# Optimization experiments

Hardware: AMD Instinct MI355X
Metric: run time of the kernel (lower is better)

Reference implementation:

```python
import jax, jax.numpy as jnp
import numpy as np

BN_EPS = 1e-5


def setup_inputs() -> dict:
    key = jax.random.key(0)
    ks = jax.random.split(key, 6)
    B, N, M, C1, C2 = 8, 8192, 2048, 128, 256
    in_ch = C1 + C2  # 384
    return {
        "xyz1": jax.random.uniform(ks[0], (B, N, 3), dtype=jnp.float32),
        "xyz2": jax.random.uniform(ks[1], (B, M, 3), dtype=jnp.float32),
        "features1": jax.random.normal(ks[2], (B, C1, N), dtype=jnp.float32),
        "features2": jax.random.normal(ks[3], (B, C2, M), dtype=jnp.float32),
        # Conv1d(kernel_size=1, bias=False) weights, squeezed to [out, in]
        "conv_w0": jax.random.normal(ks[4], (256, in_ch), dtype=jnp.float32) * 0.05,
        "gamma0": jnp.ones((256,), dtype=jnp.float32),
        "beta0": jnp.zeros((256,), dtype=jnp.float32),
        "conv_w1": jax.random.normal(ks[5], (256, 256), dtype=jnp.float32) * 0.05,
        "gamma1": jnp.ones((256,), dtype=jnp.float32),
        "beta1": jnp.zeros((256,), dtype=jnp.float32),
    }


def _conv_bn_relu(x, w, gamma, beta):
    # 1x1 Conv1d (no bias) == per-point channel matmul: [B,Cin,N] -> [B,Cout,N]
    x = jnp.einsum("oc,bcn->bon", w, x)
    # BatchNorm1d in training mode: batch stats over (B, N), biased variance
    mu = jnp.mean(x, axis=(0, 2), keepdims=True)
    var = jnp.var(x, axis=(0, 2), keepdims=True)
    x = (x - mu) * jax.lax.rsqrt(var + BN_EPS)
    x = x * gamma[None, :, None] + beta[None, :, None]
    return jax.nn.relu(x)


def reference(xyz1, xyz2, features1, features2,
              conv_w0, gamma0, beta0, conv_w1, gamma1, beta1):
    # squared pairwise distances [B, N, M] (broadcast diff reduced over coord dim)
    diff = xyz1[:, :, None, :] - xyz2[:, None, :, :]  # [B,N,M,3]
    dists = jnp.sum(diff * diff, axis=-1)             # [B,N,M]
    idx = jnp.argmin(dists, axis=-1)                  # [B,N] nearest downsampled point

    # per-batch gather: features2[b, :, idx[b]] -> [B, C2, N]
    interp = jax.vmap(lambda f, i: f[:, i])(features2, idx)

    x = jnp.concatenate([features1, interp], axis=1)  # [B, C1+C2, N]
    x = _conv_bn_relu(x, conv_w0, gamma0, beta0)
    x = _conv_bn_relu(x, conv_w1, gamma1, beta1)
    return x
```

## Files before the change

### kernel.cpp

```cpp
#include <hip/hip_runtime.h>
#include <stdint.h>

typedef unsigned short u16;
typedef unsigned int u32;
typedef __attribute__((ext_vector_type(8))) short short8;
typedef __attribute__((ext_vector_type(4))) float floatx4;

__device__ __forceinline__ u16 f2b(float f) {
  union { float f; u32 u; } c; c.f = f;
  u32 u = c.u;
  u += 0x7fffu + ((u >> 16) & 1u);
  return (u16)(u >> 16);
}
__device__ __forceinline__ float b2f(u16 h) {
  union { u32 u; float f; } c; c.u = ((u32)h) << 16;
  return c.f;
}

__device__ __forceinline__ void glds16(const void* g, void* l) {
  __builtin_amdgcn_global_load_lds((__attribute__((address_space(1))) void*)g,
                                   (__attribute__((address_space(3))) void*)l, 16, 0, 0);
}

__global__ void prep_all_k(const float* __restrict__ xyz1, const float* __restrict__ xyz2,
                           float2* __restrict__ cand,
                           const float* __restrict__ f1, u16* __restrict__ f1t,
                           const float* __restrict__ f2, u16* __restrict__ f2t,
                           const float* __restrict__ w0, u16* __restrict__ w0b,
                           const float* __restrict__ w1, u16* __restrict__ w1b,
                           float* __restrict__ sums) {
  __shared__ __align__(16) char smem[9216];
  int blk = blockIdx.x, t = threadIdx.x;
  if (blk < 512) {
    float4* s2 = (float4*)smem;
    int nq = blk & 7, mq = (blk >> 3) & 7, b = blk >> 6;
    const float* x2 = xyz2 + ((size_t)b * 2048 + mq * 256) * 3;
    s2[t] = make_float4(x2[t * 3], x2[t * 3 + 1], x2[t * 3 + 2], 0.f);
    __syncthreads();
    int n0 = nq * 1024 + t;
    float px[4], py[4], pz[4];
#pragma unroll
    for (int q = 0; q < 4; q++) {
      const float* p1 = xyz1 + ((size_t)b * 8192 + n0 + q * 256) * 3;
      px[q] = p1[0]; py[q] = p1[1]; pz[q] = p1[2];
    }
    float best[4] = {3.0e38f, 3.0e38f, 3.0e38f, 3.0e38f};
    int bi[4] = {0, 0, 0, 0};
#pragma unroll 4
    for (int m = 0; m < 256; m++) {
      float4 qq = s2[m];
#pragma unroll
      for (int q = 0; q < 4; q++) {
        float dx = px[q] - qq.x, dy = py[q] - qq.y, dz = pz[q] - qq.z;
        float d = fmaf(dz, dz, fmaf(dy, dy, dx * dx));
        bool c = d < best[q];
        best[q] = c ? d : best[q];
        bi[q] = c ? m : bi[q];
      }
    }
#pragma unroll
    for (int q = 0; q < 4; q++) {
      int n = n0 + q * 256;
      cand[(size_t)mq * 65536 + (size_t)b * 8192 + n] =
          make_float2(best[q], __int_as_float(mq * 256 + bi[q]));
    }
  } else if (blk < 3584) {
    const float* in; u16* out; int C, N, bx, by, bz;
    if (blk < 2560) { int rel = blk - 512;  in = f1; out = f1t; C = 128; N = 8192; bx = rel & 127; by = (rel >> 7) & 1; bz = rel >> 8; }
    else            { int rel = blk - 2560; in = f2; out = f2t; C = 256; N = 2048; bx = rel & 31;  by = (rel >> 5) & 3; bz = rel >> 7; }
    u16 (*tile)[72] = (u16(*)[72])smem;
    int c0 = by * 64, n0 = bx * 64;
    const float* src = in + ((size_t)bz * C + c0) * N + n0;
#pragma unroll
    for (int i = 0; i < 4; i++) {
      int id = t + i * 256;
      int c = id >> 4, nq = (id & 15) * 4;
      float4 v = *(const float4*)(src + (size_t)c * N + nq);
      tile[nq + 0][c] = f2b(v.x);
      tile[nq + 1][c] = f2b(v.y);
      tile[nq + 2][c] = f2b(v.z);
      tile[nq + 3][c] = f2b(v.w);
    }
    __syncthreads();
    int n = t >> 2, ch = (t & 3) * 16;
    u16* dst = out + ((size_t)bz * N + n0 + n) * C + c0 + ch;
    *(uint4*)dst = *(const uint4*)&tile[n][ch];
    *(uint4*)(dst + 8) = *(const uint4*)&tile[n][ch + 8];
  } else {
    int rel = blk - 3584;
    int i = rel * 256 + t;
    if (rel < 384) w0b[i] = f2b(w0[i]);
    else { int j = i - 98304; w1b[j] = f2b(w1[j]); }
    if (rel < 4) sums[i] = 0.f;
  }
}

__global__ __launch_bounds__(256, 2) void gemm1_k(const u16* __restrict__ w0b, const u16* __restrict__ f1t,
                                                  const u16* __restrict__ f2t, const float2* __restrict__ cand,
                                                  float* __restrict__ sum0, float* __restrict__ sq0,
                                                  u16* __restrict__ y0) {
  __shared__ u16 Bs[2][64 * 64];
  __shared__ float red[256];
  int t = threadIdx.x;
  int bid = blockIdx.x;
  int ohalf = (bid >> 3) & 1;
  int pairidx = (bid & 7) | ((bid >> 4) << 3);
  int o0 = ohalf * 128;
  int lane = t & 63, wave = t >> 6;
  int wrow = (wave >> 1) * 64;
  int wp = (wave & 1) * 32;
  int lr = lane & 15, lq = lane >> 4;
  int srow = lane >> 3;
  int sch = ((lane & 7) ^ srow) * 8;

  red[t] = 0.f;

  short8 areg[4][12];
#pragma unroll
  for (int i = 0; i < 4; i++) {
    const u16* wr = w0b + (size_t)(o0 + wrow + i * 16 + lr) * 384 + lq * 8;
#pragma unroll
    for (int kf = 0; kf < 12; kf++)
      areg[i][kf] = *(const short8*)(wr + kf * 32);
  }

  for (int s = 0; s < 4; s++) {
    int pt0 = (pairidx * 4 + s) * 64;
    size_t bb = (size_t)((pt0 >> 13) << 11);
    int gidx[2];
#pragma unroll
    for (int i = 0; i < 2; i++) {
      int p = pt0 + (wave * 2 + i) * 8 + srow;
      float bd = 3.0e38f; int bi = 0;
#pragma unroll
      for (int qc = 0; qc < 8; qc++) {
        float2 c = cand[(size_t)qc * 65536 + p];
        if (c.x < bd) { bd = c.x; bi = __float_as_int(c.y); }
      }
      gidx[i] = bi;
    }
    floatx4 zero = {0.f, 0.f, 0.f, 0.f};
    floatx4 acc[4][2];
#pragma unroll
    for (int i = 0; i < 4; i++)
#pragma unroll
      for (int j = 0; j < 2; j++) acc[i][j] = zero;

    auto stageB = [&](int step, int bufi) {
#pragma unroll
      for (int i = 0; i < 2; i++) {
        int row = (wave * 2 + i) * 8 + srow;
        const u16* src;
        if (step < 2) src = f1t + (size_t)(pt0 + row) * 128 + step * 64 + sch;
        else          src = f2t + (bb + gidx[i]) * 256 + (step * 64 - 128) + sch;
        glds16(src, &Bs[bufi][(wave * 2 + i) * 512]);
      }
    };

    stageB(0, 0);
    __syncthreads();
#pragma unroll
    for (int step = 0; step < 6; step++) {
      if (step < 5) stageB(step + 1, (step + 1) & 1);
#pragma unroll
      for (int ks = 0; ks < 2; ks++) {
        short8 bf[2];
#pragma unroll
        for (int j = 0; j < 2; j++)
          bf[j] = *(const short8*)&Bs[step & 1][(wp + j * 16 + lr) * 64 +
                                               ((((ks << 2) | lq) ^ (lr & 7)) << 3)];
        int kf = step * 2 + ks;
#pragma unroll
        for (int i = 0; i < 4; i++)
#pragma unroll
          for (int j = 0; j < 2; j++)
            acc[i][j] = __builtin_amdgcn_mfma_f32_16x16x32_bf16(areg[i][kf], bf[j], acc[i][j], 0, 0, 0);
      }
      __syncthreads();
    }

#pragma unroll
    for (int i = 0; i < 4; i++) {
#pragma unroll
      for (int j = 0; j < 2; j++) {
        int o = o0 + wrow + i * 16 + lq * 4;
        int p = pt0 + wp + j * 16 + lr;
        uint2 pk;
        pk.x = (u32)f2b(acc[i][j][0]) | ((u32)f2b(acc[i][j][1]) << 16);
        pk.y = (u32)f2b(acc[i][j][2]) | ((u32)f2b(acc[i][j][3]) << 16);
        *(uint2*)&y0[(size_t)p * 256 + o] = pk;
      }
#pragma unroll
      for (int r = 0; r < 4; r++) {
        float sv = acc[i][0][r] + acc[i][1][r];
        float qv = acc[i][0][r] * acc[i][0][r] + acc[i][1][r] * acc[i][1][r];
#pragma unroll
        for (int m = 8; m >= 1; m >>= 1) { sv += __shfl_xor(sv, m); qv += __shfl_xor(qv, m); }
        if (lr == 0) {
          int o = wrow + i * 16 + lq * 4 + r;
          atomicAdd(&red[o], sv);
          atomicAdd(&red[128 + o], qv);
        }
      }
    }
  }

  __syncthreads();
  if (t < 128) {
    atomicAdd(&sum0[o0 + t], red[t]);
    atomicAdd(&sq0[o0 + t], red[128 + t]);
  }
}

__global__ __launch_bounds__(512, 2) void gemm2_k(const u16* __restrict__ w1b, const u16* __restrict__ y0,
                                                  const float* __restrict__ sum0, const float* __restrict__ sq0,
                                                  const float* __restrict__ gamma0, const float* __restrict__ beta0,
                                                  float* __restrict__ sum1, float* __restrict__ sq1,
                                                  u16* __restrict__ y1) {
  __shared__ u16 Aw[128 * 256];
  __shared__ u16 Bs[2][256 * 64];
  __shared__ float ssc[256], ssh[256];
  int t = threadIdx.x;
  int bid = blockIdx.x;
  int ohalf = (bid >> 3) & 1;
  int pairidx = (bid & 7) | ((bid >> 4) << 3);
  int o0 = ohalf * 128;
  int lane = t & 63, wave = t >> 6;
  int wrow = (wave >> 2) * 64;
  int wp = (wave & 3) * 64;
  int lr = lane & 15, lq = lane >> 4;
  if (t < 256) {
    float mean = sum0[t] * (1.f / 65536.f);
    float var = fmaxf(sq0[t] * (1.f / 65536.f) - mean * mean, 0.f);
    float r = rsqrtf(var + 1e-5f);
    float sc = gamma0[t] * r;
    ssc[t] = sc;
    ssh[t] = beta0[t] - mean * sc;
  }
#pragma unroll
  for (int it = 0; it < 8; it++) {
    u32 off = (u32)it * 8192 + (u32)t * 16;
    int row = off >> 9;
    int c16 = (off & 511) >> 4;
    glds16(w1b + (size_t)(o0 + row) * 256 + ((c16 ^ (row & 7)) << 3),
           (char*)Aw + (size_t)it * 8192 + (size_t)wave * 1024);
  }

  int brow[4], bpc[4], bch[4];
#pragma unroll
  for (int i = 0; i < 4; i++) {
    int id = t + i * 512;
    brow[i] = id >> 3; bpc[i] = id & 7;
    bch[i] = (bpc[i] ^ (brow[i] & 7)) * 8;
  }
  float sa[4][4], qa[4][4];
#pragma unroll
  for (int i = 0; i < 4; i++)
#pragma unroll
    for (int r = 0; r < 4; r++) { sa[i][r] = 0.f; qa[i][r] = 0.f; }

  __syncthreads();

  for (int s = 0; s < 2; s++) {
    int pt0 = (pairidx * 2 + s) * 256;
    uint4 rg[4];
    auto loadB = [&](int k0) {
#pragma unroll
      for (int i = 0; i < 4; i++)
        rg[i] = *(const uint4*)(y0 + (size_t)(pt0 + brow[i]) * 256 + k0 + bch[i]);
    };
    auto xformB = [&](int k0, int bufi) {
#pragma unroll
      for (int i = 0; i < 4; i++) {
        u32 rw[4] = {rg[i].x, rg[i].y, rg[i].z, rg[i].w};
        u32 ow[4];
#pragma unroll
        for (int w = 0; w < 4; w++) {
          int k = k0 + bch[i] + w * 2;
          float v0 = b2f((u16)(rw[w] & 0xffffu));
          float v1 = b2f((u16)(rw[w] >> 16));
          v0 = fmaxf(v0 * ssc[k] + ssh[k], 0.f);
          v1 = fmaxf(v1 * ssc[k + 1] + ssh[k + 1], 0.f);
          ow[w] = (u32)f2b(v0) | ((u32)f2b(v1) << 16);
        }
        uint4 ov; ov.x = ow[0]; ov.y = ow[1]; ov.z = ow[2]; ov.w = ow[3];
        *(uint4*)&Bs[bufi][brow[i] * 64 + bpc[i] * 8] = ov;
      }
    };
    floatx4 zero = {0.f, 0.f, 0.f, 0.f};
    floatx4 acc[4][4];
#pragma unroll
    for (int i = 0; i < 4; i++)
#pragma unroll
      for (int j = 0; j < 4; j++) acc[i][j] = zero;
    auto compute = [&](int k0, int bufi) {
#pragma unroll
      for (int ks = 0; ks < 2; ks++) {
        short8 af[4], bf[4];
#pragma unroll
        for (int i = 0; i < 4; i++) {
          int row = wrow + i * 16 + lr;
          af[i] = *(const short8*)&Aw[row * 256 + ((((k0 >> 3) + (ks << 2) + lq) ^ (lr & 7)) << 3)];
        }
#pragma unroll
        for (int j = 0; j < 4; j++) {
          int row = wp + j * 16 + lr;
          bf[j] = *(const short8*)&Bs[bufi][row * 64 + ((((ks << 2) | lq) ^ (lr & 7)) << 3)];
        }
#pragma unroll
        for (int i = 0; i < 4; i++)
#pragma unroll
          for (int j = 0; j < 4; j++)
            acc[i][j] = __builtin_amdgcn_mfma_f32_16x16x32_bf16(af[i], bf[j], acc[i][j], 0, 0, 0);
      }
    };

    loadB(0);
    xformB(0, 0);
    __syncthreads();
#pragma unroll
    for (int k0i = 0; k0i < 4; k0i++) {
      if (k0i < 3) loadB((k0i + 1) * 64);
      compute(k0i * 64, k0i & 1);
      __syncthreads();
      if (k0i < 3) {
        xformB((k0i + 1) * 64, (k0i + 1) & 1);
        __syncthreads();
      }
    }
#pragma unroll
    for (int i = 0; i < 4; i++) {
#pragma unroll
      for (int j = 0; j < 4; j++) {
        int o = o0 + wrow + i * 16 + lq * 4;
        int p = pt0 + wp + j * 16 + lr;
        uint2 pk;
        pk.x = (u32)f2b(acc[i][j][0]) | ((u32)f2b(acc[i][j][1]) << 16);
        pk.y = (u32)f2b(acc[i][j][2]) | ((u32)f2b(acc[i][j][3]) << 16);
        *(uint2*)&y1[(size_t)p * 256 + o] = pk;
      }
#pragma unroll
      for (int r = 0; r < 4; r++) {
        float v0 = acc[i][0][r], v1 = acc[i][1][r], v2 = acc[i][2][r], v3 = acc[i][3][r];
        sa[i][r] += v0 + v1 + v2 + v3;
        qa[i][r] += v0 * v0 + v1 * v1 + v2 * v2 + v3 * v3;
      }
    }
  }

#pragma unroll
  for (int i = 0; i < 4; i++)
#pragma unroll
    for (int r = 0; r < 4; r++)
#pragma unroll
      for (int m = 8; m >= 1; m >>= 1) {
        sa[i][r] += __shfl_xor(sa[i][r], m);
        qa[i][r] += __shfl_xor(qa[i][r], m);
      }
  __syncthreads();
  float* red = (float*)&Bs[0][0];
  if (t < 256) red[t] = 0.f;
  __syncthreads();
  if (lr == 0) {
#pragma unroll
    for (int i = 0; i < 4; i++)
#pragma unroll
      for (int r = 0; r < 4; r++) {
        int o = wrow + i * 16 + lq * 4 + r;
        atomicAdd(&red[o], sa[i][r]);
        atomicAdd(&red[128 + o], qa[i][r]);
      }
  }
  __syncthreads();
  if (t < 128) {
    atomicAdd(&sum1[o0 + t], red[t]);
    atomicAdd(&sq1[o0 + t], red[128 + t]);
  }
}

__global__ void finalize_k(const u16* __restrict__ y1, const float* __restrict__ sum1,
                           const float* __restrict__ sq1, const float* __restrict__ gamma1,
                           const float* __restrict__ beta1, float* __restrict__ out) {
  __shared__ float tile[64][65];
  __shared__ float fs[64], fh[64];
  int b = blockIdx.z, o0 = blockIdx.y * 64, n0 = blockIdx.x * 64;
  int t = threadIdx.x;
  if (t < 64) {
    int o = o0 + t;
    float mean = sum1[o] * (1.f / 65536.f);
    float var = fmaxf(sq1[o] * (1.f / 65536.f) - mean * mean, 0.f);
    float r = rsqrtf(var + 1e-5f);
    float sc = gamma1[o] * r;
    fs[t] = sc;
    fh[t] = beta1[o] - mean * sc;
  }
  __syncthreads();
  int pl = t >> 2, ch = (t & 3) * 16;
  const u16* src = y1 + ((size_t)(b * 8192 + n0 + pl)) * 256 + o0 + ch;
  uint4 r0 = *(const uint4*)src;
  uint4 r1 = *(const uint4*)(src + 8);
  u16 hv[16];
  *(uint4*)&hv[0] = r0;
  *(uint4*)&hv[8] = r1;
#pragma unroll
  for (int e = 0; e < 16; e++) {
    float v = b2f(hv[e]) * fs[ch + e] + fh[ch + e];
    tile[pl][ch + e] = fmaxf(v, 0.f);
  }
  __syncthreads();
  int ol = t >> 2, nch = (t & 3) * 16;
  float* dst = out + ((size_t)(b * 256 + o0 + ol)) * 8192 + n0 + nch;
#pragma unroll
  for (int j = 0; j < 16; j += 4) {
    float4 v = make_float4(tile[nch + j][ol], tile[nch + j + 1][ol],
                           tile[nch + j + 2][ol], tile[nch + j + 3][ol]);
    *(float4*)(dst + j) = v;
  }
}

extern "C" void kernel_launch(void* const* d_in, const int* in_sizes, int n_in,
                              void* d_out, int out_size, void* d_ws, size_t ws_size,
                              hipStream_t stream) {
  const float* xyz1      = (const float*)d_in[0];
  const float* xyz2      = (const float*)d_in[1];
  const float* features1 = (const float*)d_in[2];
  const float* features2 = (const float*)d_in[3];
  const float* conv_w0   = (const float*)d_in[4];
  const float* gamma0    = (const float*)d_in[5];
  const float* beta0     = (const float*)d_in[6];
  const float* conv_w1   = (const float*)d_in[7];
  const float* gamma1    = (const float*)d_in[8];
  const float* beta1     = (const float*)d_in[9];
  float* out = (float*)d_out;

  char* ws = (char*)d_ws;
  size_t off = 0;
  auto alloc = [&](size_t bytes) {
    char* p = ws + off;
    off = (off + bytes + 4095) & ~(size_t)4095;
    return p;
  };
  float*  sums = (float*)alloc(4 * 256 * 4);
  u16*    w0b  = (u16*)alloc(256 * 384 * 2);
  u16*    w1b  = (u16*)alloc(256 * 256 * 2);
  float2* cand = (float2*)alloc((size_t)8 * 65536 * 8);
  u16*    f1t  = (u16*)alloc((size_t)65536 * 128 * 2);
  u16*    f2t  = (u16*)alloc((size_t)16384 * 256 * 2);
  u16*    y0   = (u16*)alloc((size_t)65536 * 256 * 2);
  u16*    y1   = (u16*)alloc((size_t)65536 * 256 * 2);

  prep_all_k<<<dim3(4224), 256, 0, stream>>>(xyz1, xyz2, cand, features1, f1t,
                                             features2, f2t, conv_w0, w0b, conv_w1, w1b, sums);
  gemm1_k<<<dim3(512), 256, 0, stream>>>(w0b, f1t, f2t, cand, sums + 0, sums + 256, y0);
  gemm2_k<<<dim3(256), 512, 0, stream>>>(w1b, y0, sums + 0, sums + 256, gamma0, beta0,
                                         sums + 512, sums + 768, y1);
  finalize_k<<<dim3(128, 4, 8), 256, 0, stream>>>(y1, sums + 512, sums + 768, gamma1, beta1, out);
}
```

Measured before the change: 247.1 us.

## Retile gemm1 with LDS-staged weights and deepen gemm2 load pipeline

gemm1 no longer holds a 128-row weight slice in registers across four point sub-tiles. Each block now stages a 64x384 weight slice in LDS through direct global-to-LDS loads and processes one 128-point tile, and the grid grows from 512 to 2048 blocks. This is meant to cut register pressure and raise parallelism, at the cost of reloading weights per block and more atomics on the BN statistics. gemm2 double-buffers its register prefetch so global loads run two K-steps ahead, and its launch bound drops to one block per CU to allow more registers.

```diff
diff --git a/kernel.cpp b/kernel.cpp
--- a/kernel.cpp
+++ b/kernel.cpp
@@ -99,120 +99,123 @@
                                                   const u16* __restrict__ f2t, const float2* __restrict__ cand,
                                                   float* __restrict__ sum0, float* __restrict__ sq0,
                                                   u16* __restrict__ y0) {
-  __shared__ u16 Bs[2][64 * 64];
-  __shared__ float red[256];
+  __shared__ u16 Aw[64 * 384];
+  __shared__ u16 Bs[2][128 * 64];
+  __shared__ float red[128];
   int t = threadIdx.x;
   int bid = blockIdx.x;
-  int ohalf = (bid >> 3) & 1;
-  int pairidx = (bid & 7) | ((bid >> 4) << 3);
-  int o0 = ohalf * 128;
+  int oq = (bid >> 3) & 3;
+  int ptile = ((bid >> 5) << 3) + (bid & 7);
+  int o0 = oq * 64;
+  int pt0 = ptile * 128;
+  int b = pt0 >> 13;
   int lane = t & 63, wave = t >> 6;
-  int wrow = (wave >> 1) * 64;
-  int wp = (wave & 1) * 32;
+  int wp = wave * 32;
   int lr = lane & 15, lq = lane >> 4;
   int srow = lane >> 3;
   int sch = ((lane & 7) ^ srow) * 8;
 
-  red[t] = 0.f;
-
-  short8 areg[4][12];
+  if (t < 128) red[t] = 0.f;
+
+#pragma unroll
+  for (int it = 0; it < 12; it++) {
+    u32 off = (u32)it * 4096 + (u32)t * 16;
+    int row = off / 768;
+    int c16 = (off - row * 768) >> 4;
+    glds16(w0b + (size_t)(o0 + row) * 384 + ((c16 ^ (row & 7)) << 3),
+           (char*)Aw + (size_t)it * 4096 + (size_t)wave * 1024);
+  }
+
+  int gidx[4];
 #pragma unroll
   for (int i = 0; i < 4; i++) {
-    const u16* wr = w0b + (size_t)(o0 + wrow + i * 16 + lr) * 384 + lq * 8;
-#pragma unroll
-    for (int kf = 0; kf < 12; kf++)
-      areg[i][kf] = *(const short8*)(wr + kf * 32);
-  }
-
-  for (int s = 0; s < 4; s++) {
-    int pt0 = (pairidx * 4 + s) * 64;
-    size_t bb = (size_t)((pt0 >> 13) << 11);
-    int gidx[2];
-#pragma unroll
-    for (int i = 0; i < 2; i++) {
-      int p = pt0 + (wave * 2 + i) * 8 + srow;
-      float bd = 3.0e38f; int bi = 0;
-#pragma unroll
-      for (int qc = 0; qc < 8; qc++) {
-        float2 c = cand[(size_t)qc * 65536 + p];
-        if (c.x < bd) { bd = c.x; bi = __float_as_int(c.y); }
-      }
-      gidx[i] = bi;
-    }
-    floatx4 zero = {0.f, 0.f, 0.f, 0.f};
-    floatx4 acc[4][2];
-#pragma unroll
-    for (int i = 0; i < 4; i++)
-#pragma unroll
-      for (int j = 0; j < 2; j++) acc[i][j] = zero;
-
-    auto stageB = [&](int step, int bufi) {
-#pragma unroll
-      for (int i = 0; i < 2; i++) {
-        int row = (wave * 2 + i) * 8 + srow;
-        const u16* src;
-        if (step < 2) src = f1t + (size_t)(pt0 + row) * 128 + step * 64 + sch;
-        else          src = f2t + (bb + gidx[i]) * 256 + (step * 64 - 128) + sch;
-        glds16(src, &Bs[bufi][(wave * 2 + i) * 512]);
-      }
-    };
-
-    stageB(0, 0);
-    __syncthreads();
-#pragma unroll
-    for (int step = 0; step < 6; step++) {
-      if (step < 5) stageB(step + 1, (step + 1) & 1);
-#pragma unroll
-      for (int ks = 0; ks < 2; ks++) {
-        short8 bf[2];
+    int p = pt0 + (wave * 4 + i) * 8 + srow;
+    float bd = 3.0e38f; int bi = 0;
+#pragma unroll
+    for (int qc = 0; qc < 8; qc++) {
+      float2 c = cand[(size_t)qc * 65536 + p];
+      if (c.x < bd) { bd = c.x; bi = __float_as_int(c.y); }
+    }
+    gidx[i] = bi;
+  }
+
+  floatx4 zero = {0.f, 0.f, 0.f, 0.f};
+  floatx4 acc[4][2];
+#pragma unroll
+  for (int i = 0; i < 4; i++)
+#pragma unroll
+    for (int j = 0; j < 2; j++) acc[i][j] = zero;
+
+  auto stageB = [&](int step, int bufi) {
+#pragma unroll
+    for (int i = 0; i < 4; i++) {
+      int row = (wave * 4 + i) * 8 + srow;
+      const u16* src;
+      if (step < 2) src = f1t + (size_t)(pt0 + row) * 128 + step * 64 + sch;
+      else          src = f2t + ((size_t)(b << 11) + gidx[i]) * 256 + (step * 64 - 128) + sch;
+      glds16(src, &Bs[bufi][(wave * 4 + i) * 512]);
+    }
+  };
+
+  stageB(0, 0);
+  __syncthreads();
+#pragma unroll
+  for (int step = 0; step < 6; step++) {
+    if (step < 5) stageB(step + 1, (step + 1) & 1);
+#pragma unroll
+    for (int ks = 0; ks < 2; ks++) {
+      short8 af[4], bf[2];
+#pragma unroll
+      for (int i = 0; i < 4; i++) {
+        int row = i * 16 + lr;
+        af[i] = *(const short8*)&Aw[row * 384 + (((step * 8 + (ks << 2) + lq) ^ (lr & 7)) << 3)];
+      }
+#pragma unroll
+      for (int j = 0; j < 2; j++) {
+        int row = wp + j * 16 + lr;
+        bf[j] = *(const short8*)&Bs[step & 1][row * 64 + ((((ks << 2) | lq) ^ (lr & 7)) << 3)];
+      }
+#pragma unroll
+      for (int i = 0; i < 4; i++)
 #pragma unroll
         for (int j = 0; j < 2; j++)
-          bf[j] = *(const short8*)&Bs[step & 1][(wp + j * 16 + lr) * 64 +
-                                               ((((ks << 2) | lq) ^ (lr & 7)) << 3)];
-        int kf = step * 2 + ks;
-#pragma unroll
-        for (int i = 0; i < 4; i++)
-#pragma unroll
-          for (int j = 0; j < 2; j++)
-            acc[i][j] = __builtin_amdgcn_mfma_f32_16x16x32_bf16(areg[i][kf], bf[j], acc[i][j], 0, 0, 0);
-      }
-      __syncthreads();
-    }
-
-#pragma unroll
-    for (int i = 0; i < 4; i++) {
-#pragma unroll
-      for (int j = 0; j < 2; j++) {
-        int o = o0 + wrow + i * 16 + lq * 4;
-        int p = pt0 + wp + j * 16 + lr;
-        uint2 pk;
-        pk.x = (u32)f2b(acc[i][j][0]) | ((u32)f2b(acc[i][j][1]) << 16);
-        pk.y = (u32)f2b(acc[i][j][2]) | ((u32)f2b(acc[i][j][3]) << 16);
-        *(uint2*)&y0[(size_t)p * 256 + o] = pk;
-      }
-#pragma unroll
-      for (int r = 0; r < 4; r++) {
-        float sv = acc[i][0][r] + acc[i][1][r];
-        float qv = acc[i][0][r] * acc[i][0][r] + acc[i][1][r] * acc[i][1][r];
-#pragma unroll
-        for (int m = 8; m >= 1; m >>= 1) { sv += __shfl_xor(sv, m); qv += __shfl_xor(qv, m); }
-        if (lr == 0) {
-          int o = wrow + i * 16 + lq * 4 + r;
-          atomicAdd(&red[o], sv);
-          atomicAdd(&red[128 + o], qv);
-        }
-      }
-    }
-  }
-
-  __syncthreads();
-  if (t < 128) {
+          acc[i][j] = __builtin_amdgcn_mfma_f32_16x16x32_bf16(af[i], bf[j], acc[i][j], 0, 0, 0);
+    }
+    __syncthreads();
+  }
+
+#pragma unroll
+  for (int i = 0; i < 4; i++) {
+#pragma unroll
+    for (int j = 0; j < 2; j++) {
+      int o = o0 + i * 16 + lq * 4;
+      int p = pt0 + wp + j * 16 + lr;
+      uint2 pk;
+      pk.x = (u32)f2b(acc[i][j][0]) | ((u32)f2b(acc[i][j][1]) << 16);
+      pk.y = (u32)f2b(acc[i][j][2]) | ((u32)f2b(acc[i][j][3]) << 16);
+      *(uint2*)&y0[(size_t)p * 256 + o] = pk;
+    }
+#pragma unroll
+    for (int r = 0; r < 4; r++) {
+      float sv = acc[i][0][r] + acc[i][1][r];
+      float qv = acc[i][0][r] * acc[i][0][r] + acc[i][1][r] * acc[i][1][r];
+#pragma unroll
+      for (int m = 8; m >= 1; m >>= 1) { sv += __shfl_xor(sv, m); qv += __shfl_xor(qv, m); }
+      if (lr == 0) {
+        int o = i * 16 + lq * 4 + r;
+        atomicAdd(&red[o], sv);
+        atomicAdd(&red[64 + o], qv);
+      }
+    }
+  }
+  __syncthreads();
+  if (t < 64) {
     atomicAdd(&sum0[o0 + t], red[t]);
-    atomicAdd(&sq0[o0 + t], red[128 + t]);
-  }
-}
-
-__global__ __launch_bounds__(512, 2) void gemm2_k(const u16* __restrict__ w1b, const u16* __restrict__ y0,
+    atomicAdd(&sq0[o0 + t], red[64 + t]);
+  }
+}
+
+__global__ __launch_bounds__(512, 1) void gemm2_k(const u16* __restrict__ w1b, const u16* __restrict__ y0,
                                                   const float* __restrict__ sum0, const float* __restrict__ sq0,
                                                   const float* __restrict__ gamma0, const float* __restrict__ beta0,
                                                   float* __restrict__ sum1, float* __restrict__ sq1,
@@ -261,73 +264,78 @@
 
   __syncthreads();
 
+  uint4 rg0[4], rg1[4];
+  auto loadB = [&](int pt0, int k0, uint4* rg) {
+#pragma unroll
+    for (int i = 0; i < 4; i++)
+      rg[i] = *(const uint4*)(y0 + (size_t)(pt0 + brow[i]) * 256 + k0 + bch[i]);
+  };
+  auto xformB = [&](int k0, const uint4* rg, int bufi) {
+#pragma unroll
+    for (int i = 0; i < 4; i++) {
+      u32 rw[4] = {rg[i].x, rg[i].y, rg[i].z, rg[i].w};
+      u32 ow[4];
+#pragma unroll
+      for (int w = 0; w < 4; w++) {
+        int k = k0 + bch[i] + w * 2;
+        float v0 = b2f((u16)(rw[w] & 0xffffu));
+        float v1 = b2f((u16)(rw[w] >> 16));
+        v0 = fmaxf(v0 * ssc[k] + ssh[k], 0.f);
+        v1 = fmaxf(v1 * ssc[k + 1] + ssh[k + 1], 0.f);
+        ow[w] = (u32)f2b(v0) | ((u32)f2b(v1) << 16);
+      }
+      uint4 ov; ov.x = ow[0]; ov.y = ow[1]; ov.z = ow[2]; ov.w = ow[3];
+      *(uint4*)&Bs[bufi][brow[i] * 64 + bpc[i] * 8] = ov;
+    }
+  };
+  floatx4 acc[4][4];
+  auto compute = [&](int k0, int bufi) {
+#pragma unroll
+    for (int ks = 0; ks < 2; ks++) {
+      short8 af[4], bf[4];
+#pragma unroll
+      for (int i = 0; i < 4; i++) {
+        int row = wrow + i * 16 + lr;
+        af[i] = *(const short8*)&Aw[row * 256 + ((((k0 >> 3) + (ks << 2) + lq) ^ (lr & 7)) << 3)];
+      }
+#pragma unroll
+      for (int j = 0; j < 4; j++) {
+        int row = wp + j * 16 + lr;
+        bf[j] = *(const short8*)&Bs[bufi][row * 64 + ((((ks << 2) | lq) ^ (lr & 7)) << 3)];
+      }
+#pragma unroll
+      for (int i = 0; i < 4; i++)
+#pragma unroll
+        for (int j = 0; j < 4; j++)
+          acc[i][j] = __builtin_amdgcn_mfma_f32_16x16x32_bf16(af[i], bf[j], acc[i][j], 0, 0, 0);
+    }
+  };
+
   for (int s = 0; s < 2; s++) {
     int pt0 = (pairidx * 2 + s) * 256;
-    uint4 rg[4];
-    auto loadB = [&](int k0) {
-#pragma unroll
-      for (int i = 0; i < 4; i++)
-        rg[i] = *(const uint4*)(y0 + (size_t)(pt0 + brow[i]) * 256 + k0 + bch[i]);
-    };
-    auto xformB = [&](int k0, int bufi) {
-#pragma unroll
-      for (int i = 0; i < 4; i++) {
-        u32 rw[4] = {rg[i].x, rg[i].y, rg[i].z, rg[i].w};
-        u32 ow[4];
-#pragma unroll
-        for (int w = 0; w < 4; w++) {
-          int k = k0 + bch[i] + w * 2;
-          float v0 = b2f((u16)(rw[w] & 0xffffu));
-          float v1 = b2f((u16)(rw[w] >> 16));
-          v0 = fmaxf(v0 * ssc[k] + ssh[k], 0.f);
-          v1 = fmaxf(v1 * ssc[k + 1] + ssh[k + 1], 0.f);
-          ow[w] = (u32)f2b(v0) | ((u32)f2b(v1) << 16);
-        }
-        uint4 ov; ov.x = ow[0]; ov.y = ow[1]; ov.z = ow[2]; ov.w = ow[3];
-        *(uint4*)&Bs[bufi][brow[i] * 64 + bpc[i] * 8] = ov;
-      }
-    };
     floatx4 zero = {0.f, 0.f, 0.f, 0.f};
-    floatx4 acc[4][4];
 #pragma unroll
     for (int i = 0; i < 4; i++)
 #pragma unroll
       for (int j = 0; j < 4; j++) acc[i][j] = zero;
-    auto compute = [&](int k0, int bufi) {
-#pragma unroll
-      for (int ks = 0; ks < 2; ks++) {
-        short8 af[4], bf[4];
-#pragma unroll
-        for (int i = 0; i < 4; i++) {
-          int row = wrow + i * 16 + lr;
-          af[i] = *(const short8*)&Aw[row * 256 + ((((k0 >> 3) + (ks << 2) + lq) ^ (lr & 7)) << 3)];
-        }
-#pragma unroll
-        for (int j = 0; j < 4; j++) {
-          int row = wp + j * 16 + lr;
-          bf[j] = *(const short8*)&Bs[bufi][row * 64 + ((((ks << 2) | lq) ^ (lr & 7)) << 3)];
-        }
-#pragma unroll
-        for (int i = 0; i < 4; i++)
-#pragma unroll
-          for (int j = 0; j < 4; j++)
-            acc[i][j] = __builtin_amdgcn_mfma_f32_16x16x32_bf16(af[i], bf[j], acc[i][j], 0, 0, 0);
-      }
-    };
-
-    loadB(0);
-    xformB(0, 0);
-    __syncthreads();
-#pragma unroll
-    for (int k0i = 0; k0i < 4; k0i++) {
-      if (k0i < 3) loadB((k0i + 1) * 64);
-      compute(k0i * 64, k0i & 1);
-      __syncthreads();
-      if (k0i < 3) {
-        xformB((k0i + 1) * 64, (k0i + 1) & 1);
-        __syncthreads();
-      }
-    }
+
+    loadB(pt0, 0, rg0);
+    xformB(0, rg0, 0);
+    loadB(pt0, 64, rg1);
+    __syncthreads();
+    loadB(pt0, 128, rg0);
+    xformB(64, rg1, 1);
+    compute(0, 0);
+    __syncthreads();
+    loadB(pt0, 192, rg1);
+    xformB(128, rg0, 0);
+    compute(64, 1);
+    __syncthreads();
+    xformB(192, rg1, 1);
+    compute(128, 0);
+    __syncthreads();
+    compute(192, 1);
+
 #pragma unroll
     for (int i = 0; i < 4; i++) {
 #pragma unroll
@@ -346,6 +354,7 @@
         qa[i][r] += v0 * v0 + v1 * v1 + v2 * v2 + v3 * v3;
       }
     }
+    __syncthreads();
   }
 
 #pragma unroll
@@ -451,7 +460,7 @@
 
   prep_all_k<<<dim3(4224), 256, 0, stream>>>(xyz1, xyz2, cand, features1, f1t,
                                              features2, f2t, conv_w0, w0b, conv_w1, w1b, sums);
-  gemm1_k<<<dim3(512), 256, 0, stream>>>(w0b, f1t, f2t, cand, sums + 0, sums + 256, y0);
+  gemm1_k<<<dim3(2048), 256, 0, stream>>>(w0b, f1t, f2t, cand, sums + 0, sums + 256, y0);
   gemm2_k<<<dim3(256), 512, 0, stream>>>(w1b, y0, sums + 0, sums + 256, gamma0, beta0,
                                          sums + 512, sums + 768, y1);
   finalize_k<<<dim3(128, 4, 8), 256, 0, stream>>>(y1, sums + 512, sums + 768, gamma1, beta1, out);
```

New measurement: 296.1 us. 1.2x slower.
